# Kernel optimization log

Measured on AMD Instinct MI355X. Metric: run time of the kernel, lower is better.

The kernel has to match this reference:

```python
import jax, jax.numpy as jnp
import numpy as np

VOX = 0.1
XMIN, YMIN, ZMIN = -20.0, -20.0, -2.0
XMAX, YMAX, ZMAX = 20.0, 20.0, 3.0
GX, GY = 400, 400          # grid size from (40m / 0.1m)
P = 32                     # max_points_per_voxel
K = 60000                  # max_num_voxels
N = 2_000_000              # total points
B = 4                      # batch size
SUB = 120                  # points drawn from a 120x120 sub-grid so uniques (<=57600) <= K


def setup_inputs() -> dict:
    key = jax.random.key(0)
    kb, kx, ky, kz, ki, ku, kv = jax.random.split(key, 7)
    b = jax.random.randint(kb, (N,), 0, B).astype(jnp.float32)
    xi = jax.random.randint(kx, (N,), 0, SUB).astype(jnp.float32)
    yi = jax.random.randint(ky, (N,), 0, SUB).astype(jnp.float32)
    ux = jax.random.uniform(ku, (N,))
    uy = jax.random.uniform(kv, (N,))
    x = XMIN + (xi + ux * 0.999) * VOX
    y = YMIN + (yi + uy * 0.999) * VOX
    z = jax.random.uniform(kz, (N,), minval=ZMIN, maxval=ZMAX - 1e-3)
    r = jax.random.uniform(ki, (N,))
    points = jnp.stack([b, x, y, z, r], axis=1)  # [N,5]
    return {"points": points, "batch_size": B}


def reference(points, batch_size):
    # in-range mask (identity for our generated data, but kept for fidelity)
    mask = ((points[:, 1] >= XMIN) & (points[:, 1] < XMAX)
            & (points[:, 2] >= YMIN) & (points[:, 2] < YMAX)
            & (points[:, 3] >= ZMIN) & (points[:, 3] < ZMAX))
    bi = points[:, 0].astype(jnp.int32)
    xi = jnp.clip(((points[:, 1] - XMIN) / VOX).astype(jnp.int32), 0, GX - 1)
    yi = jnp.clip(((points[:, 2] - YMIN) / VOX).astype(jnp.int32), 0, GY - 1)
    # flat voxel id; numeric order == lexicographic (b,x,y) order as in torch.unique(dim=0)
    flat = bi * (GX * GY) + xi * GY + yi
    sentinel = jnp.int32(batch_size * GX * GY)
    flat = jnp.where(mask, flat, sentinel)
    uniq, inv = jnp.unique(flat, size=K, fill_value=sentinel, return_inverse=True)
    inv = inv.astype(jnp.int32)

    # points per voxel (clamped to slot capacity)
    counts = jax.ops.segment_sum(mask.astype(jnp.int32), inv, num_segments=K)
    counts = jnp.minimum(counts, P)

    # slot = rank of each point within its voxel, in original point order
    order = jnp.argsort(inv)                      # stable
    sinv = inv[order]
    first = jnp.searchsorted(sinv, sinv, side='left')
    ranks = (jnp.arange(N) - first).astype(jnp.int32)
    slot = jnp.zeros(N, jnp.int32).at[order].set(ranks)

    # scatter point features into fixed-size voxel slots; overflow/out-of-range dropped
    rows = jnp.where(mask, inv, K)                # K is OOB -> dropped
    voxels = jnp.zeros((K, P, 4), points.dtype).at[rows, slot].set(
        points[:, 1:5], mode='drop')

    # decode sorted unique flat ids back to (batch, x, y)
    cb = uniq // (GX * GY)
    rem = uniq % (GX * GY)
    coors = jnp.stack([cb, rem // GY, rem % GY], axis=1)
    return voxels, counts, coors
```

## Files before the change

### kernel.cpp

```cpp
#include <hip/hip_runtime.h>

namespace {

constexpr int GX = 400, GY = 400;
constexpr int P = 32;
constexpr int K = 60000;
constexpr int MCAP = 128;
constexpr int NB = 4;
constexpr int NVOX = NB * GX * GY;
constexpr int SCAN_CHUNK = 1024;
constexpr int NBLK = (NVOX + 1 + SCAN_CHUNK - 1) / SCAN_CHUNK;
constexpr int OCC_PAD = NBLK * SCAN_CHUNK;

constexpr unsigned A20 = 0x779B1u;
constexpr unsigned mulinv20(unsigned a) {
  unsigned x = a;
  for (int i = 0; i < 6; ++i) x *= 2u - a * x;
  return x & 0xFFFFFu;
}
constexpr unsigned AINV20 = mulinv20(A20);
static_assert(((A20 * AINV20) & 0xFFFFFu) == 1u, "bad inverse");

constexpr int NBUK3 = 512;
constexpr int JH = 2048;
constexpr int CAP3 = 5120;
constexpr int PPB3 = 2048;

constexpr float XMINf = -20.f, YMINf = -20.f, ZMINf = -2.f;
constexpr float XMAXf =  20.f, YMAXf =  20.f, ZMAXf =  3.f;

constexpr int OUT_CNT = K * P * 4;
constexpr int OUT_COR = OUT_CNT + K;

typedef float floatx2 __attribute__((ext_vector_type(2)));

__device__ __forceinline__ int bin_of(float v) {
  return (int)((v + 20.0f) * 10.0f);
}

__device__ __forceinline__ bool point_voxel(const float* __restrict__ pt, int& flat) {
  float x = pt[1], y = pt[2], z = pt[3];
  bool m = (x >= XMINf) & (x < XMAXf) & (y >= YMINf) & (y < YMAXf)
         & (z >= ZMINf) & (z < ZMAXf);
  if (!m) return false;
  int bi = (int)pt[0];
  int xi = min(max(bin_of(x), 0), GX - 1);
  int yi = min(max(bin_of(y), 0), GY - 1);
  flat = bi * (GX * GY) + xi * GY + yi;
  return true;
}

__device__ __forceinline__ unsigned bf16rne(float f) {
  unsigned u = __float_as_uint(f);
  return ((u + 0x7fffu + ((u >> 16) & 1u)) >> 16) & 0xffffu;
}
__device__ __forceinline__ float bf16dq(unsigned h) {
  return __uint_as_float(h << 16);
}

__global__ void __launch_bounds__(256) k_mark_bucket(
    const float* __restrict__ pts, int n, int* __restrict__ occ,
    int* __restrict__ bcur, unsigned* __restrict__ akey,
    uint2* __restrict__ afeat) {
  __shared__ int hist[512], lb[512], gb[512], ofs[512];
  __shared__ unsigned stk[PPB3];
  __shared__ uint2 stf[PPB3];
  __shared__ unsigned short stb[PPB3];
  __shared__ int ps[256];
  __shared__ int tot_s;
  int t = threadIdx.x;
  for (int j = t; j < 512; j += 256) hist[j] = 0;
  __syncthreads();

  int base = blockIdx.x * PPB3;
  int bk[8]; unsigned rec[8]; uint2 ft[8];
  #pragma unroll
  for (int j = 0; j < 8; ++j) {
    int i = base + j * 256 + t;
    bk[j] = -1;
    if (i < n) {
      const float* pp = pts + (size_t)i * 5;
      int flat;
      if (point_voxel(pp, flat)) {
        occ[flat] = 1;
        unsigned u = ((unsigned)flat * A20) & 0xFFFFFu;
        bk[j] = (int)(u >> 11);
        rec[j] = ((u & 0x7FFu) << 21) | (unsigned)i;
        ft[j].x = bf16rne(pp[1]) | (bf16rne(pp[2]) << 16);
        ft[j].y = bf16rne(pp[3]) | (bf16rne(pp[4]) << 16);
      }
    }
    if (bk[j] >= 0) atomicAdd(&hist[bk[j]], 1);
  }
  __syncthreads();
  int h0 = hist[2 * t], h1 = hist[2 * t + 1];
  int local = h0 + h1;
  ps[t] = local;
  __syncthreads();
  for (int o = 1; o < 256; o <<= 1) {
    int add = (t >= o) ? ps[t - o] : 0;
    __syncthreads();
    ps[t] += add;
    __syncthreads();
  }
  int excl = ps[t] - local;
  lb[2 * t] = excl;          ofs[2 * t] = excl;
  lb[2 * t + 1] = excl + h0; ofs[2 * t + 1] = excl + h0;
  if (t == 255) tot_s = ps[255];
  __syncthreads();
  #pragma unroll
  for (int j = 0; j < 8; ++j) {
    if (bk[j] >= 0) {
      int pos = atomicAdd(&ofs[bk[j]], 1);
      stk[pos] = rec[j];
      stf[pos] = ft[j];
      stb[pos] = (unsigned short)bk[j];
    }
  }
  __syncthreads();
  for (int b = t; b < NBUK3; b += 256) {
    int nb = hist[b];
    gb[b] = nb ? atomicAdd(&bcur[b], nb) : 0;
  }
  __syncthreads();
  int tot = tot_s;
  for (int e = t; e < tot; e += 256) {
    int b = stb[e];
    int dst = gb[b] + (e - lb[b]);
    if (dst < CAP3) {
      akey[(size_t)b * CAP3 + dst] = stk[e];
      afeat[(size_t)b * CAP3 + dst] = stf[e];
    }
  }
}

__global__ void k_bsum(const int* __restrict__ occ, int* __restrict__ bsum) {
  __shared__ int wsums[4];
  int t = threadIdx.x, wid = t >> 6, lane = t & 63;
  int base = blockIdx.x * SCAN_CHUNK;
  int4 v = ((const int4*)(occ + base))[t];
  int s = v.x + v.y + v.z + v.w;
  for (int o = 32; o > 0; o >>= 1) s += __shfl_xor(s, o, 64);
  if (lane == 0) wsums[wid] = s;
  __syncthreads();
  if (t == 0) bsum[blockIdx.x] = wsums[0] + wsums[1] + wsums[2] + wsums[3];
}

__global__ void k_scanb(int* __restrict__ bsum) {
  __shared__ int lds[1024];
  int t = threadIdx.x;
  int v = (t < NBLK) ? bsum[t] : 0;
  lds[t] = v;
  __syncthreads();
  for (int o = 1; o < 1024; o <<= 1) {
    int add = (t >= o) ? lds[t - o] : 0;
    __syncthreads();
    lds[t] += add;
    __syncthreads();
  }
  if (t < NBLK) bsum[t] = lds[t] - v;
  if (t == NBLK - 1) bsum[NBLK] = lds[t];
}

__global__ void k_rank(int* __restrict__ occ, const int* __restrict__ bsum,
                       int* __restrict__ uniq) {
  __shared__ int wsums[4];
  int t = threadIdx.x, wid = t >> 6, lane = t & 63;
  int base = blockIdx.x * SCAN_CHUNK;
  int4 v = ((const int4*)(occ + base))[t];
  int tsum = v.x + v.y + v.z + v.w;
  int sc = tsum;
  for (int o = 1; o < 64; o <<= 1) {
    int u = __shfl_up(sc, o, 64);
    if (lane >= o) sc += u;
  }
  if (lane == 63) wsums[wid] = sc;
  __syncthreads();
  int woff = 0;
  for (int w = 0; w < wid; ++w) woff += wsums[w];
  int p = bsum[blockIdx.x] + woff + (sc - tsum);
  int e0 = base + t * 4;
  int4 r;
  r.x = p; if (v.x) { if (p < K) uniq[p] = e0 + 0; ++p; }
  r.y = p; if (v.y) { if (p < K) uniq[p] = e0 + 1; ++p; }
  r.z = p; if (v.z) { if (p < K) uniq[p] = e0 + 2; ++p; }
  r.w = p; if (v.w) { if (p < K) uniq[p] = e0 + 3; ++p; }
  ((int4*)(occ + base))[t] = r;
}

__global__ void __launch_bounds__(256) k_build2(
    unsigned* __restrict__ akey, unsigned short* __restrict__ gpos,
    const int* __restrict__ bcur, const int* __restrict__ rank,
    const int* __restrict__ nuq_p, int* __restrict__ voxoff,
    int* __restrict__ vcnt) {
  __shared__ unsigned st[CAP3];
  __shared__ int hist[JH], scn[JH], cur[JH];
  __shared__ int ps[256];
  int b = blockIdx.x, t = threadIdx.x;
  int tot = min(bcur[b], CAP3);
  for (int j = t; j < JH; j += 256) hist[j] = 0;
  __syncthreads();
  unsigned* keys = akey + (size_t)b * CAP3;
  for (int i = t; i < tot; i += 256) {
    unsigned kk = keys[i];
    st[i] = kk;
    atomicAdd(&hist[kk >> 21], 1);
  }
  __syncthreads();
  int h[8]; int local = 0;
  #pragma unroll
  for (int u = 0; u < 8; ++u) { h[u] = hist[8 * t + u]; local += h[u]; }
  ps[t] = local;
  __syncthreads();
  for (int o = 1; o < 256; o <<= 1) {
    int add = (t >= o) ? ps[t - o] : 0;
    __syncthreads();
    ps[t] += add;
    __syncthreads();
  }
  int run = ps[t] - local;
  #pragma unroll
  for (int u = 0; u < 8; ++u) { scn[8 * t + u] = run; cur[8 * t + u] = run; run += h[u]; }
  __syncthreads();
  int cbase = b * CAP3;
  for (int i = t; i < tot; i += 256) {
    unsigned kk = st[i];
    int slot = atomicAdd(&cur[kk >> 21], 1);
    keys[slot] = kk & 0x1FFFFFu;
    gpos[cbase + slot] = (unsigned short)i;
  }
  int nq = min(nuq_p[0], K);
  for (int j = t; j < JH; j += 256) {
    if (hist[j] > 0) {
      unsigned u = ((unsigned)b << 11) | (unsigned)j;
      int flat = (int)((u * AINV20) & 0xFFFFFu);
      int k = rank[flat];
      if (k >= 0 && k < nq) {
        voxoff[k] = cbase + scn[j];
        vcnt[k] = hist[j];
      }
    }
  }
}

__global__ void __launch_bounds__(256) k_final_g(
    const unsigned* __restrict__ akey, const unsigned short* __restrict__ gpos,
    const uint2* __restrict__ afeat, const int* __restrict__ uniq,
    const int* __restrict__ voxoff, const int* __restrict__ vcnt,
    const int* __restrict__ nuq_p, float* __restrict__ out) {
  int wid = threadIdx.x >> 6, lane = threadIdx.x & 63;
  int k = blockIdx.x * 4 + wid;
  if (k >= K) return;
  int nq = min(nuq_p[0], K);
  const unsigned UMAX = 0xffffffffu;
  int s = lane >> 1, hh = lane & 1;

  int c_tot = 0, c_out = 0, off = 0;
  if (k < nq) {
    off = voxoff[k];
    int c = vcnt[k];
    c_tot = min(c, MCAP);
    c_out = min(c, P);
  }

  unsigned pos_s = 0u;
  if (c_tot > 0) {
    if (c_tot <= 64) {
      unsigned key = (lane < c_tot) ? akey[off + lane] : UMAX;
      unsigned pos = (lane < c_tot) ? (unsigned)gpos[off + lane] : 0u;
      for (int kk = 2; kk <= 64; kk <<= 1) {
        for (int d = kk >> 1; d >= 1; d >>= 1) {
          unsigned pk = __shfl_xor(key, d, 64);
          unsigned pq = __shfl_xor(pos, d, 64);
          bool tmin = ((lane & d) == 0) == ((lane & kk) == 0);
          bool sw = tmin ? (pk < key) : (pk > key);
          if (sw) { key = pk; pos = pq; }
        }
      }
      pos_s = __shfl(pos, s, 64);
    } else {
      unsigned k0 = (lane < c_tot) ? akey[off + lane] : UMAX;
      unsigned p0 = (lane < c_tot) ? (unsigned)gpos[off + lane] : 0u;
      unsigned k1 = (lane + 64 < c_tot) ? akey[off + 64 + lane] : UMAX;
      unsigned p1 = (lane + 64 < c_tot) ? (unsigned)gpos[off + 64 + lane] : 0u;
      #pragma unroll
      for (int ph = 1; ph <= 7; ++ph) {
        int kk = 1 << ph;
        bool up = ((lane & (kk >> 1)) == 0);
        #pragma unroll
        for (int d = kk >> 1; d >= 2; d >>= 1) {
          int dl = d >> 1;
          unsigned q0 = __shfl_xor(k0, dl, 64), r0 = __shfl_xor(p0, dl, 64);
          unsigned q1 = __shfl_xor(k1, dl, 64), r1 = __shfl_xor(p1, dl, 64);
          bool low = ((lane & dl) == 0);
          if (low == up) {
            if (q0 < k0) { k0 = q0; p0 = r0; }
            if (q1 < k1) { k1 = q1; p1 = r1; }
          } else {
            if (q0 > k0) { k0 = q0; p0 = r0; }
            if (q1 > k1) { k1 = q1; p1 = r1; }
          }
        }
        bool sw = up ? (k1 < k0) : (k1 > k0);
        if (sw) {
          unsigned tk = k0; k0 = k1; k1 = tk;
          unsigned tp = p0; p0 = p1; p1 = tp;
        }
      }
      unsigned a0 = __shfl(p0, s >> 1, 64);
      unsigned a1 = __shfl(p1, s >> 1, 64);
      pos_s = (s & 1) ? a1 : a0;
    }
  }

  uint2 fv = make_uint2(0u, 0u);
  if (s < c_out) {
    int b = off / CAP3;
    fv = afeat[(size_t)b * CAP3 + pos_s];
  }
  float va, vb;
  if (hh == 0) { va = bf16dq(fv.x & 0xffffu); vb = bf16dq(fv.x >> 16); }
  else         { va = bf16dq(fv.y & 0xffffu); vb = bf16dq(fv.y >> 16); }
  floatx2 val = {va, vb};
  __builtin_nontemporal_store(val, (floatx2*)(out + (size_t)k * (P * 4)) + lane);

  if (lane == 0) {
    out[OUT_CNT + k] = (float)c_out;
    int f = (k < nq) ? uniq[k] : NVOX;
    int cb = f / (GX * GY), rem = f % (GX * GY);
    out[OUT_COR + (size_t)k * 3 + 0] = (float)cb;
    out[OUT_COR + (size_t)k * 3 + 1] = (float)(rem / GY);
    out[OUT_COR + (size_t)k * 3 + 2] = (float)(rem % GY);
  }
}

__global__ void k_mark(const float* __restrict__ pts, int n,
                       int* __restrict__ occ, int* __restrict__ pflat) {
  int i = blockIdx.x * blockDim.x + threadIdx.x;
  if (i >= n) return;
  int flat = -1;
  if (point_voxel(pts + (size_t)i * 5, flat)) occ[flat] = 1;
  if (pflat) pflat[i] = flat;
}

__global__ void k_append(const int* __restrict__ pflat, int n,
                         const int* __restrict__ rank, int* __restrict__ cnt,
                         unsigned* __restrict__ vox) {
  int i = blockIdx.x * blockDim.x + threadIdx.x;
  if (i >= n) return;
  int f = pflat[i];
  if (f < 0) return;
  int v = rank[f];
  if (v >= K) return;
  int pos = atomicAdd(&cnt[v], 1);
  if (pos < MCAP) vox[(size_t)v * MCAP + pos] = (unsigned)i;
}

__global__ void k_append_fb(const float* __restrict__ pts, int n,
                            const int* __restrict__ rank, int* __restrict__ cnt,
                            unsigned* __restrict__ vox) {
  int i = blockIdx.x * blockDim.x + threadIdx.x;
  if (i >= n) return;
  int flat;
  if (!point_voxel(pts + (size_t)i * 5, flat)) return;
  int v = rank[flat];
  if (v >= K) return;
  int pos = atomicAdd(&cnt[v], 1);
  if (pos < MCAP) vox[(size_t)v * MCAP + pos] = (unsigned)i;
}

__global__ void __launch_bounds__(256) k_final_d(
    const float* __restrict__ pts, const int* __restrict__ uniq,
    const int* __restrict__ cnt, const int* __restrict__ nuq_p,
    float* __restrict__ out) {
  int wid = threadIdx.x >> 6, lane = threadIdx.x & 63;
  int k = blockIdx.x * 4 + wid;
  if (k >= K) return;
  int nuq = min(nuq_p[0], K);
  int c_tot = 0, c_out = 0;
  if (k < nuq) {
    int c = cnt[k];
    c_tot = min(c, MCAP);
    c_out = min(c, P);
  }
  const unsigned UMAX = 0xffffffffu;
  const unsigned* row = (const unsigned*)out + (size_t)k * MCAP;
  uint2 q = ((const uint2*)row)[lane];
  unsigned v0 = (2 * lane     < c_tot) ? q.x : UMAX;
  unsigned v1 = (2 * lane + 1 < c_tot) ? q.y : UMAX;
  #pragma unroll
  for (int ph = 1; ph <= 7; ++ph) {
    int kk = 1 << ph;
    bool up = ((lane & (kk >> 1)) == 0);
    #pragma unroll
    for (int d = kk >> 1; d >= 2; d >>= 1) {
      int dl = d >> 1;
      unsigned p0 = __shfl_xor(v0, dl, 64);
      unsigned p1 = __shfl_xor(v1, dl, 64);
      bool low = ((lane & dl) == 0);
      if (low == up) { v0 = min(v0, p0); v1 = min(v1, p1); }
      else           { v0 = max(v0, p0); v1 = max(v1, p1); }
    }
    unsigned lo = min(v0, v1), hi = max(v0, v1);
    v0 = up ? lo : hi;
    v1 = up ? hi : lo;
  }
  int mys = lane >> 1, h = lane & 1;
  unsigned a0 = __shfl(v0, mys >> 1, 64);
  unsigned a1 = __shfl(v1, mys >> 1, 64);
  unsigned myidx = (mys & 1) ? a1 : a0;
  float a = 0.f, b = 0.f;
  if (mys < c_out) {
    const float* pp = pts + (size_t)myidx * 5;
    a = pp[1 + 2 * h];
    b = pp[2 + 2 * h];
  }
  float2* vout = (float2*)(out + (size_t)k * (P * 4));
  vout[lane] = make_float2(a, b);
  if (lane == 0) {
    out[OUT_CNT + k] = (float)c_out;
    int f = (k < nuq) ? uniq[k] : NVOX;
    int cb = f / (GX * GY), rem = f % (GX * GY);
    out[OUT_COR + (size_t)k * 3 + 0] = (float)cb;
    out[OUT_COR + (size_t)k * 3 + 1] = (float)(rem / GY);
    out[OUT_COR + (size_t)k * 3 + 2] = (float)(rem % GY);
  }
}

}

extern "C" void kernel_launch(void* const* d_in, const int* in_sizes, int n_in,
                              void* d_out, int out_size, void* d_ws, size_t ws_size,
                              hipStream_t stream) {
  const float* pts = (const float*)d_in[0];
  int n = in_sizes[0] / 5;
  float* out = (float*)d_out;
  int nb_pts = (n + 255) / 256;

  size_t o_occ   = 0;
  size_t o_bsum  = o_occ + OCC_PAD;
  size_t o_uniq  = o_bsum + NBLK + 1;
  size_t o_voff  = o_uniq + K;
  size_t o_vcnt  = o_voff + K;
  size_t o_bcur  = o_vcnt + K;
  size_t o_akey  = (o_bcur + NBUK3 + 3) & ~(size_t)3;
  size_t o_afeat = o_akey + (size_t)NBUK3 * CAP3;
  size_t o_gpos  = o_afeat + (size_t)NBUK3 * CAP3 * 2;
  size_t totA    = o_gpos + ((size_t)NBUK3 * CAP3 + 1) / 2;

  if (ws_size >= totA * sizeof(int) && n <= (1 << 21)) {
    int* occ   = (int*)d_ws + o_occ;
    int* bsum  = (int*)d_ws + o_bsum;
    int* uniq  = (int*)d_ws + o_uniq;
    int* voff  = (int*)d_ws + o_voff;
    int* vcnt  = (int*)d_ws + o_vcnt;
    int* bcur  = (int*)d_ws + o_bcur;
    unsigned* akey = (unsigned*)((int*)d_ws + o_akey);
    uint2* afeat   = (uint2*)((int*)d_ws + o_afeat);
    unsigned short* gpos = (unsigned short*)((int*)d_ws + o_gpos);
    const int* nuq_p = bsum + NBLK;

    hipMemsetAsync(occ, 0, (size_t)OCC_PAD * sizeof(int), stream);
    hipMemsetAsync(bcur, 0, (size_t)NBUK3 * sizeof(int), stream);
    k_mark_bucket<<<(n + PPB3 - 1) / PPB3, 256, 0, stream>>>(pts, n, occ, bcur, akey, afeat);
    k_bsum  <<<NBLK, 256, 0, stream>>>(occ, bsum);
    k_scanb <<<1, 1024, 0, stream>>>(bsum);
    k_rank  <<<NBLK, 256, 0, stream>>>(occ, bsum, uniq);
    k_build2<<<NBUK3, 256, 0, stream>>>(akey, gpos, bcur, occ, nuq_p, voff, vcnt);
    k_final_g<<<(K + 3) / 4, 256, 0, stream>>>(akey, gpos, afeat, uniq, voff, vcnt, nuq_p, out);
  } else {
    int* occ  = (int*)d_ws;
    int* bsum = occ + OCC_PAD;
    int* uniq = bsum + (NBLK + 1);
    int* cnt  = uniq + K;
    size_t base_ints = (size_t)OCC_PAD + (NBLK + 1) + K + K;
    base_ints = (base_ints + 3) & ~(size_t)3;
    int* pflat = (int*)d_ws + base_ints;
    bool use_pflat = ws_size >= (base_ints + (size_t)n) * sizeof(int);

    hipMemsetAsync(occ, 0, (size_t)OCC_PAD * sizeof(int), stream);
    hipMemsetAsync(cnt, 0, (size_t)K * sizeof(int), stream);
    k_mark  <<<nb_pts, 256, 0, stream>>>(pts, n, occ, use_pflat ? pflat : nullptr);
    k_bsum  <<<NBLK, 256, 0, stream>>>(occ, bsum);
    k_scanb <<<1, 1024, 0, stream>>>(bsum);
    k_rank  <<<NBLK, 256, 0, stream>>>(occ, bsum, uniq);
    if (use_pflat)
      k_append<<<nb_pts, 256, 0, stream>>>(pflat, n, occ, cnt, (unsigned*)out);
    else
      k_append_fb<<<nb_pts, 256, 0, stream>>>(pts, n, occ, cnt, (unsigned*)out);
    k_final_d<<<(K + 3) / 4, 256, 0, stream>>>(pts, uniq, cnt, bsum + NBLK, out);
  }
}
```

Measured before the change: 145.3 us.

## Replace block-local LDS bucketing with direct per-partition global atomic scatter

The point-bucketing kernel no longer builds a per-block histogram, scan and LDS staging area. Each thread now handles four consecutive points and appends each one directly to one of 512×8 partitioned global buckets using a global atomic counter. The build kernel is adapted to gather the eight partition segments per bucket and to record source offsets that account for the partition layout. This removes the block-level syncs and LDS traffic, but every point now costs a global atomic and a scattered, uncoalesced write. Each partition is also capped at 640 entries, which could overflow on skewed inputs.

```diff
diff --git a/kernel.cpp b/kernel.cpp
--- a/kernel.cpp
+++ b/kernel.cpp
@@ -22,9 +22,10 @@
 static_assert(((A20 * AINV20) & 0xFFFFFu) == 1u, "bad inverse");
 
 constexpr int NBUK3 = 512;
+constexpr int NPART = 8;
+constexpr int CAPS = 640;
+constexpr int CAP3 = NPART * CAPS;
 constexpr int JH = 2048;
-constexpr int CAP3 = 5120;
-constexpr int PPB3 = 2048;
 
 constexpr float XMINf = -20.f, YMINf = -20.f, ZMINf = -2.f;
 constexpr float XMAXf =  20.f, YMAXf =  20.f, ZMAXf =  3.f;
@@ -58,78 +59,30 @@
   return __uint_as_float(h << 16);
 }
 
-__global__ void __launch_bounds__(256) k_mark_bucket(
+__global__ void __launch_bounds__(256) k_scatter(
     const float* __restrict__ pts, int n, int* __restrict__ occ,
-    int* __restrict__ bcur, unsigned* __restrict__ akey,
+    int* __restrict__ bcur2, unsigned* __restrict__ akey,
     uint2* __restrict__ afeat) {
-  __shared__ int hist[512], lb[512], gb[512], ofs[512];
-  __shared__ unsigned stk[PPB3];
-  __shared__ uint2 stf[PPB3];
-  __shared__ unsigned short stb[PPB3];
-  __shared__ int ps[256];
-  __shared__ int tot_s;
-  int t = threadIdx.x;
-  for (int j = t; j < 512; j += 256) hist[j] = 0;
-  __syncthreads();
-
-  int base = blockIdx.x * PPB3;
-  int bk[8]; unsigned rec[8]; uint2 ft[8];
+  int part = blockIdx.x & (NPART - 1);
+  int base = (blockIdx.x * 256 + threadIdx.x) * 4;
   #pragma unroll
-  for (int j = 0; j < 8; ++j) {
-    int i = base + j * 256 + t;
-    bk[j] = -1;
-    if (i < n) {
-      const float* pp = pts + (size_t)i * 5;
-      int flat;
-      if (point_voxel(pp, flat)) {
-        occ[flat] = 1;
-        unsigned u = ((unsigned)flat * A20) & 0xFFFFFu;
-        bk[j] = (int)(u >> 11);
-        rec[j] = ((u & 0x7FFu) << 21) | (unsigned)i;
-        ft[j].x = bf16rne(pp[1]) | (bf16rne(pp[2]) << 16);
-        ft[j].y = bf16rne(pp[3]) | (bf16rne(pp[4]) << 16);
+  for (int j = 0; j < 4; ++j) {
+    int i = base + j;
+    if (i >= n) break;
+    const float* pp = pts + (size_t)i * 5;
+    int flat;
+    if (point_voxel(pp, flat)) {
+      occ[flat] = 1;
+      unsigned u = ((unsigned)flat * A20) & 0xFFFFFu;
+      int b = (int)(u >> 11);
+      unsigned key = ((u & 0x7FFu) << 21) | (unsigned)i;
+      int pos = atomicAdd(&bcur2[b * NPART + part], 1);
+      if (pos < CAPS) {
+        size_t a = (size_t)(b * NPART + part) * CAPS + pos;
+        akey[a] = key;
+        afeat[a] = make_uint2(bf16rne(pp[1]) | (bf16rne(pp[2]) << 16),
+                              bf16rne(pp[3]) | (bf16rne(pp[4]) << 16));
       }
-    }
-    if (bk[j] >= 0) atomicAdd(&hist[bk[j]], 1);
-  }
-  __syncthreads();
-  int h0 = hist[2 * t], h1 = hist[2 * t + 1];
-  int local = h0 + h1;
-  ps[t] = local;
-  __syncthreads();
-  for (int o = 1; o < 256; o <<= 1) {
-    int add = (t >= o) ? ps[t - o] : 0;
-    __syncthreads();
-    ps[t] += add;
-    __syncthreads();
-  }
-  int excl = ps[t] - local;
-  lb[2 * t] = excl;          ofs[2 * t] = excl;
-  lb[2 * t + 1] = excl + h0; ofs[2 * t + 1] = excl + h0;
-  if (t == 255) tot_s = ps[255];
-  __syncthreads();
-  #pragma unroll
-  for (int j = 0; j < 8; ++j) {
-    if (bk[j] >= 0) {
-      int pos = atomicAdd(&ofs[bk[j]], 1);
-      stk[pos] = rec[j];
-      stf[pos] = ft[j];
-      stb[pos] = (unsigned short)bk[j];
-    }
-  }
-  __syncthreads();
-  for (int b = t; b < NBUK3; b += 256) {
-    int nb = hist[b];
-    gb[b] = nb ? atomicAdd(&bcur[b], nb) : 0;
-  }
-  __syncthreads();
-  int tot = tot_s;
-  for (int e = t; e < tot; e += 256) {
-    int b = stb[e];
-    int dst = gb[b] + (e - lb[b]);
-    if (dst < CAP3) {
-      akey[(size_t)b * CAP3 + dst] = stk[e];
-      afeat[(size_t)b * CAP3 + dst] = stf[e];
     }
   }
 }
@@ -190,21 +143,33 @@
 
 __global__ void __launch_bounds__(256) k_build2(
     unsigned* __restrict__ akey, unsigned short* __restrict__ gpos,
-    const int* __restrict__ bcur, const int* __restrict__ rank,
+    const int* __restrict__ bcur2, const int* __restrict__ rank,
     const int* __restrict__ nuq_p, int* __restrict__ voxoff,
     int* __restrict__ vcnt) {
   __shared__ unsigned st[CAP3];
   __shared__ int hist[JH], scn[JH], cur[JH];
   __shared__ int ps[256];
+  __shared__ int segb[NPART + 1];
   int b = blockIdx.x, t = threadIdx.x;
-  int tot = min(bcur[b], CAP3);
   for (int j = t; j < JH; j += 256) hist[j] = 0;
+  if (t == 0) {
+    int run = 0;
+    for (int s = 0; s < NPART; ++s) {
+      segb[s] = run;
+      run += min(bcur2[b * NPART + s], CAPS);
+    }
+    segb[NPART] = run;
+  }
   __syncthreads();
   unsigned* keys = akey + (size_t)b * CAP3;
-  for (int i = t; i < tot; i += 256) {
-    unsigned kk = keys[i];
-    st[i] = kk;
-    atomicAdd(&hist[kk >> 21], 1);
+  for (int s = 0; s < NPART; ++s) {
+    int c = segb[s + 1] - segb[s];
+    const unsigned* seg = akey + ((size_t)b * NPART + s) * CAPS;
+    for (int i = t; i < c; i += 256) {
+      unsigned kk = seg[i];
+      st[segb[s] + i] = kk;
+      atomicAdd(&hist[kk >> 21], 1);
+    }
   }
   __syncthreads();
   int h[8]; int local = 0;
@@ -222,12 +187,17 @@
   #pragma unroll
   for (int u = 0; u < 8; ++u) { scn[8 * t + u] = run; cur[8 * t + u] = run; run += h[u]; }
   __syncthreads();
+  int tot = segb[NPART];
   int cbase = b * CAP3;
-  for (int i = t; i < tot; i += 256) {
-    unsigned kk = st[i];
+  for (int e = t; e < tot; e += 256) {
+    unsigned kk = st[e];
+    int s = 0;
+    #pragma unroll
+    for (int q = 1; q < NPART; ++q) s += (e >= segb[q]);
+    int srcoff = s * CAPS + (e - segb[s]);
     int slot = atomicAdd(&cur[kk >> 21], 1);
     keys[slot] = kk & 0x1FFFFFu;
-    gpos[cbase + slot] = (unsigned short)i;
+    gpos[cbase + slot] = (unsigned short)srcoff;
   }
   int nq = min(nuq_p[0], K);
   for (int j = t; j < JH; j += 256) {
@@ -443,7 +413,7 @@
   size_t o_voff  = o_uniq + K;
   size_t o_vcnt  = o_voff + K;
   size_t o_bcur  = o_vcnt + K;
-  size_t o_akey  = (o_bcur + NBUK3 + 3) & ~(size_t)3;
+  size_t o_akey  = (o_bcur + NBUK3 * NPART + 3) & ~(size_t)3;
   size_t o_afeat = o_akey + (size_t)NBUK3 * CAP3;
   size_t o_gpos  = o_afeat + (size_t)NBUK3 * CAP3 * 2;
   size_t totA    = o_gpos + ((size_t)NBUK3 * CAP3 + 1) / 2;
@@ -454,19 +424,20 @@
     int* uniq  = (int*)d_ws + o_uniq;
     int* voff  = (int*)d_ws + o_voff;
     int* vcnt  = (int*)d_ws + o_vcnt;
-    int* bcur  = (int*)d_ws + o_bcur;
+    int* bcur2 = (int*)d_ws + o_bcur;
     unsigned* akey = (unsigned*)((int*)d_ws + o_akey);
     uint2* afeat   = (uint2*)((int*)d_ws + o_afeat);
     unsigned short* gpos = (unsigned short*)((int*)d_ws + o_gpos);
     const int* nuq_p = bsum + NBLK;
 
     hipMemsetAsync(occ, 0, (size_t)OCC_PAD * sizeof(int), stream);
-    hipMemsetAsync(bcur, 0, (size_t)NBUK3 * sizeof(int), stream);
-    k_mark_bucket<<<(n + PPB3 - 1) / PPB3, 256, 0, stream>>>(pts, n, occ, bcur, akey, afeat);
+    hipMemsetAsync(bcur2, 0, (size_t)NBUK3 * NPART * sizeof(int), stream);
+    int nb_sc = (n + 1023) / 1024;
+    k_scatter<<<nb_sc, 256, 0, stream>>>(pts, n, occ, bcur2, akey, afeat);
     k_bsum  <<<NBLK, 256, 0, stream>>>(occ, bsum);
     k_scanb <<<1, 1024, 0, stream>>>(bsum);
     k_rank  <<<NBLK, 256, 0, stream>>>(occ, bsum, uniq);
-    k_build2<<<NBUK3, 256, 0, stream>>>(akey, gpos, bcur, occ, nuq_p, voff, vcnt);
+    k_build2<<<NBUK3, 256, 0, stream>>>(akey, gpos, bcur2, occ, nuq_p, voff, vcnt);
     k_final_g<<<(K + 3) / 4, 256, 0, stream>>>(akey, gpos, afeat, uniq, voff, vcnt, nuq_p, out);
   } else {
     int* occ  = (int*)d_ws;
```

Measured after the change: 244.8 us. 1.68x slower.
